# Optimization experiments

Measured on AMD Instinct MI355X. Metric: run time of the kernel, lower is better.

## Reference

```python
import jax, jax.numpy as jnp
import numpy as np

N = 100000
F_IN = 128
HIDDEN = 64
HEADS = 4
EPS = 1e-16
SLOPE = 0.2  # PyG GATConv default negative_slope


def gat_conv(x, src, dst, W, a_src, a_dst, b, heads, out_ch, concat, n_nodes):
    # x: [N, F]; W: [F, heads*out_ch]; a_src/a_dst: [heads, out_ch]
    h = (x @ W).reshape(n_nodes, heads, out_ch)              # [N, H, C]
    alpha_s = jnp.einsum('nhc,hc->nh', h, a_src)             # [N, H]
    alpha_d = jnp.einsum('nhc,hc->nh', h, a_dst)             # [N, H]
    e = alpha_s[src] + alpha_d[dst]                          # [E, H]
    e = jnp.where(e > 0, e, SLOPE * e)                       # leaky_relu
    # segment softmax over destination node
    m = jax.ops.segment_max(e, dst, num_segments=n_nodes)    # [N, H]
    m = jnp.where(jnp.isfinite(m), m, 0.0)                   # empty segments
    ex = jnp.exp(e - m[dst])                                 # [E, H]
    denom = jax.ops.segment_sum(ex, dst, num_segments=n_nodes)  # [N, H]
    alpha = ex / (denom[dst] + EPS)                          # [E, H]
    # weighted scatter-aggregate of source features at destinations
    msg = h[src] * alpha[:, :, None]                         # [E, H, C]
    out = jax.ops.segment_sum(msg, dst, num_segments=n_nodes)  # [N, H, C]
    if concat:
        out = out.reshape(n_nodes, heads * out_ch)
    else:
        out = out.mean(axis=1)
    return out + b


def setup_inputs() -> dict:
    key = jax.random.key(0)
    ks = jax.random.split(key, 12)
    x = jax.random.normal(ks[0], (N, F_IN), dtype=jnp.float32)
    edge_index = jax.random.randint(ks[1], (2, 1600000), 0, N, dtype=jnp.int64)
    s1 = 1.0 / np.sqrt(F_IN)
    s2 = 1.0 / np.sqrt(HIDDEN)
    return {
        'x': x,
        'edge_index': edge_index,
        'W1': jax.random.normal(ks[2], (F_IN, HIDDEN), dtype=jnp.float32) * s1,
        'a_src1': jax.random.normal(ks[3], (HEADS, HIDDEN // HEADS), dtype=jnp.float32) * s2,
        'a_dst1': jax.random.normal(ks[4], (HEADS, HIDDEN // HEADS), dtype=jnp.float32) * s2,
        'b1': jnp.zeros((HIDDEN,), dtype=jnp.float32),
        'W2': jax.random.normal(ks[5], (HIDDEN, HIDDEN), dtype=jnp.float32) * s2,
        'a_src2': jax.random.normal(ks[6], (1, HIDDEN), dtype=jnp.float32) * s2,
        'a_dst2': jax.random.normal(ks[7], (1, HIDDEN), dtype=jnp.float32) * s2,
        'b2': jnp.zeros((HIDDEN,), dtype=jnp.float32),
        'Wc': jax.random.normal(ks[8], (HIDDEN, 1), dtype=jnp.float32) * s2,
        'bc': jnp.zeros((1,), dtype=jnp.float32),
    }


def reference(x, edge_index, W1, a_src1, a_dst1, b1, W2, a_src2, a_dst2, b2, Wc, bc):
    src, dst = edge_index[0], edge_index[1]
    # dropout layers are identity in eval mode
    h = gat_conv(x, src, dst, W1, a_src1, a_dst1, b1,
                 heads=HEADS, out_ch=HIDDEN // HEADS, concat=True, n_nodes=N)
    h = jax.nn.relu(h)
    h = gat_conv(h, src, dst, W2, a_src2, a_dst2, b2,
                 heads=1, out_ch=HIDDEN, concat=False, n_nodes=N)
    h = jax.nn.relu(h)
    return h @ Wc + bc  # [N, 1]
```

## Files before the change

kernel.cpp:

```cpp
#include <hip/hip_runtime.h>
#include <hip/hip_bf16.h>


typedef __hip_bfloat16 bf16;
typedef unsigned short ushort;
typedef unsigned char uchar;
typedef __attribute__((ext_vector_type(8))) short short8;
typedef __attribute__((ext_vector_type(4))) float f32x4;

#define NN 100000
#define EE 1600000
#define BKB 9
#define BKN (1 << BKB)
#define NBK ((NN + BKN - 1) >> BKB)
#define CAP 10240
#define TILE 4096
#define EPT 16
#define NT ((EE + TILE - 1) / TILE)
#define GP 391
#define BN 16
#define CHE 512
#define NGRP (NN / BN)

__device__ __forceinline__ float relu_np(float v) { return (v < 0.f) ? 0.f : v; }
__device__ __forceinline__ float lrelu(float v) { return v > 0.f ? v : 0.2f * v; }
__device__ __forceinline__ ushort f2bf(float f) {
    __hip_bfloat16 h = __float2bfloat16(f);
    return *reinterpret_cast<ushort*>(&h);
}
__device__ __forceinline__ float bf2f(ushort u) {
    unsigned int x = ((unsigned int)u) << 16;
    return __uint_as_float(x);
}

__global__ __launch_bounds__(256) void k_pt(
    const int* __restrict__ src, const int* __restrict__ dst,
    int* __restrict__ gcur, int* __restrict__ pairs,
    const float* __restrict__ W1,
    const float* __restrict__ aS1, const float* __restrict__ aD1,
    const float* __restrict__ W2, const float* __restrict__ aS2,
    const float* __restrict__ aD2,
    ushort* __restrict__ wB16, ushort* __restrict__ wE16,
    ushort* __restrict__ wExt)
{
    __shared__ int lh[4][NBK];
    const int bid = blockIdx.x;
    const int tid = threadIdx.x;

    if (bid < NT) {
        for (int i = tid; i < 4 * NBK; i += 256) ((int*)lh)[i] = 0;
        __syncthreads();
        const int wv = tid >> 6;
        const int e0 = bid * TILE;
        int pk[EPT], bk[EPT], rv[EPT];
        #pragma unroll
        for (int j = 0; j < EPT; ++j) {
            int e = e0 + j * 256 + tid;
            if (e < EE) {
                int d = dst[e];
                bk[j] = d >> BKB;
                pk[j] = src[e] | ((d & (BKN - 1)) << 17);
                rv[j] = atomicAdd(&lh[wv][bk[j]], 1);
            }
        }
        __syncthreads();
        for (int i = tid; i < NBK; i += 256) {
            int c0 = lh[0][i], c1 = lh[1][i], c2 = lh[2][i], c3 = lh[3][i];
            int tot = c0 + c1 + c2 + c3;
            int b = tot ? atomicAdd(&gcur[i], tot) : 0;
            lh[0][i] = b;
            lh[1][i] = b + c0;
            lh[2][i] = b + c0 + c1;
            lh[3][i] = b + c0 + c1 + c2;
        }
        __syncthreads();
        #pragma unroll
        for (int j = 0; j < EPT; ++j) {
            int e = e0 + j * 256 + tid;
            if (e < EE)
                pairs[(size_t)bk[j] * CAP + lh[wv][bk[j]] + rv[j]] = pk[j];
        }
    } else if (bid == NT) {
        for (int i = tid; i < 128 * 64; i += 256) {
            int k = i >> 6, n = i & 63;
            wB16[n * 128 + k] = f2bf(W1[i]);
        }
        for (int i = tid; i < 128 * 16; i += 256) {
            int k = i >> 4, j = i & 15;
            float v = 0.f;
            if (j < 8) {
                int h = j & 3;
                const float* av = (j < 4) ? aS1 : aD1;
                for (int c = 0; c < 16; ++c)
                    v = fmaf(W1[k * 64 + h * 16 + c], av[h * 16 + c], v);
            }
            wE16[j * 128 + k] = f2bf(v);
        }
    } else {
        for (int i = tid; i < 80 * 64; i += 256) {
            int n = i >> 6, k = i & 63;
            float v = 0.f;
            if (n < 64) {
                v = W2[k * 64 + n];
            } else if (n == 64) {
                for (int c = 0; c < 64; ++c) v = fmaf(W2[k * 64 + c], aS2[c], v);
            } else if (n == 65) {
                for (int c = 0; c < 64; ++c) v = fmaf(W2[k * 64 + c], aD2[c], v);
            }
            wExt[i] = f2bf(v);
        }
    }
}

__global__ __launch_bounds__(256) void k_bgg(
    const int* __restrict__ gcur, const int* __restrict__ pairs,
    int* __restrict__ row_ptr, uchar* __restrict__ rcnt,
    int* __restrict__ col,
    const float* __restrict__ x,
    const ushort* __restrict__ wB16, const ushort* __restrict__ wE16,
    ushort* __restrict__ h1, float* __restrict__ as1, float* __restrict__ ad1)
{
    __shared__ int h4[4][BKN];
    __shared__ int sP[256];
    const int bid = blockIdx.x;
    const int tid = threadIdx.x;

    if (bid >= NBK) {
        const int gb = bid - NBK;
        const int w = tid >> 6, lane = tid & 63;
        const int m = lane & 15, quad = lane >> 4;
        const int ntiles = NN >> 4;
        for (int tile = gb * 4 + w; tile < ntiles; tile += GP * 4) {
            const int row0 = tile << 4;
            f32x4 acc[4] = {f32x4{0,0,0,0}, f32x4{0,0,0,0},
                            f32x4{0,0,0,0}, f32x4{0,0,0,0}};
            f32x4 acc5 = {0, 0, 0, 0};
            const float* xp = x + (size_t)(row0 + m) * 128 + quad * 8;
            #pragma unroll
            for (int ks = 0; ks < 128; ks += 32) {
                f32x4 x0 = *(const f32x4*)(xp + ks);
                f32x4 x1 = *(const f32x4*)(xp + ks + 4);
                short8 a;
                #pragma unroll
                for (int j = 0; j < 4; ++j) a[j] = (short)f2bf(x0[j]);
                #pragma unroll
                for (int j = 0; j < 4; ++j) a[4 + j] = (short)f2bf(x1[j]);
                #pragma unroll
                for (int t = 0; t < 4; ++t) {
                    short8 b = *(const short8*)&wB16[(t * 16 + m) * 128 + ks + quad * 8];
                    acc[t] = __builtin_amdgcn_mfma_f32_16x16x32_bf16(a, b, acc[t], 0, 0, 0);
                }
                short8 b5 = *(const short8*)&wE16[m * 128 + ks + quad * 8];
                acc5 = __builtin_amdgcn_mfma_f32_16x16x32_bf16(a, b5, acc5, 0, 0, 0);
            }
            #pragma unroll
            for (int t = 0; t < 4; ++t)
                #pragma unroll
                for (int r = 0; r < 4; ++r)
                    h1[(size_t)(row0 + quad * 4 + r) * 64 + t * 16 + m] = f2bf(acc[t][r]);
            #pragma unroll
            for (int r = 0; r < 4; ++r) {
                int row = row0 + quad * 4 + r;
                if (m < 4) as1[row * 4 + m] = acc5[r];
                else if (m < 8) ad1[row * 4 + (m - 4)] = acc5[r];
            }
        }
        return;
    }

    const int b = bid;
    const int n0 = b << BKB;
    const int wv = tid >> 6;
    const int base = b * CAP, endE = base + gcur[b];

    for (int i = tid; i < 4 * BKN; i += 256) ((int*)h4)[i] = 0;
    __syncthreads();
    for (int i = base + tid; i < endE; i += 256)
        atomicAdd(&h4[wv][pairs[i] >> 17], 1);
    __syncthreads();

    const int na = 2 * tid, nb2 = 2 * tid + 1;
    int c00 = h4[0][na], c01 = h4[1][na], c02 = h4[2][na], c03 = h4[3][na];
    int c10 = h4[0][nb2], c11 = h4[1][nb2], c12 = h4[2][nb2], c13 = h4[3][nb2];
    int a0 = c00 + c01 + c02 + c03;
    int a1 = c10 + c11 + c12 + c13;
    int tot = a0 + a1;
    sP[tid] = tot;
    __syncthreads();
    for (int off = 1; off < 256; off <<= 1) {
        int t = (tid >= off) ? sP[tid - off] : 0;
        __syncthreads();
        sP[tid] += t;
        __syncthreads();
    }
    const int excl = sP[tid] - tot;
    const int c0 = base + excl;
    const int c1 = c0 + a0;
    if (n0 + na < NN) {
        row_ptr[n0 + na] = c0;
        rcnt[n0 + na] = (uchar)a0;
    }
    if (n0 + nb2 < NN) {
        row_ptr[n0 + nb2] = c1;
        rcnt[n0 + nb2] = (uchar)a1;
    }
    h4[0][na] = c0;
    h4[1][na] = c0 + c00;
    h4[2][na] = c0 + c00 + c01;
    h4[3][na] = c0 + c00 + c01 + c02;
    h4[0][nb2] = c1;
    h4[1][nb2] = c1 + c10;
    h4[2][nb2] = c1 + c10 + c11;
    h4[3][nb2] = c1 + c10 + c11 + c12;
    __syncthreads();
    for (int i = base + tid; i < endE; i += 256) {
        int pr = pairs[i];
        int p = atomicAdd(&h4[wv][pr >> 17], 1);
        col[p] = pr & 0x1FFFF;
    }
}

__global__ __launch_bounds__(256, 8) void k_seg1f(
    const int* __restrict__ rp, const uchar* __restrict__ rcnt,
    const int* __restrict__ col,
    const float* __restrict__ as1, const float* __restrict__ ad1,
    const ushort* __restrict__ h1, const float* __restrict__ b1,
    const ushort* __restrict__ wExt,
    ushort* __restrict__ h2, float* __restrict__ as2, float* __restrict__ ad2)
{
    __shared__ __align__(16) ushort zS[BN * 72];
    __shared__ float pS[CHE * 4];
    __shared__ int colS[CHE];
    __shared__ uchar ndS[CHE];
    __shared__ int sRp[BN + 1];
    __shared__ float bS[64];
    __shared__ float adS[BN * 4];

    const int tid = threadIdx.x;
    const int n0 = blockIdx.x * BN;

    if (tid < 64) bS[tid] = b1[tid];
    if (tid < BN * 4) adS[tid] = ad1[(size_t)n0 * 4 + tid];
    if (tid < BN) sRp[tid] = rp[n0 + tid];
    if (tid == BN) sRp[BN] = rp[n0 + BN - 1] + (int)rcnt[n0 + BN - 1];
    __syncthreads();

    const int eb0 = sRp[0];
    const int cnt = min(sRp[BN] - eb0, CHE);

    for (int t = tid; t < cnt; t += 256) {
        int ge = eb0 + t;
        colS[t] = col[ge];
        int nd = 0;
        #pragma unroll
        for (int k = 1; k < BN; ++k) nd += (ge >= sRp[k]);
        ndS[t] = (uchar)nd;
    }
    __syncthreads();
    for (int t = tid; t < cnt * 4; t += 256) {
        int e = t >> 2, hh = t & 3;
        float v = as1[(size_t)colS[e] * 4 + hh] + adS[ndS[e] * 4 + hh];
        pS[t] = __expf(lrelu(v));
    }
    __syncthreads();

    const int w = tid >> 6, lane = tid & 63;
    const int g = lane >> 4, c4 = lane & 15, head = c4 >> 2;
    const int nb = w * 4 + g;
    const int s_n = sRp[nb] - eb0, e_n = sRp[nb + 1] - eb0;

    f32x4 acc = {0, 0, 0, 0};
    float den = 0.f;
    int i = s_n;
    for (; i + 3 < e_n; i += 4) {
        int cA = colS[i], cB = colS[i + 1], cC = colS[i + 2], cD = colS[i + 3];
        ushort4 hA = *(const ushort4*)&h1[(size_t)cA * 64 + c4 * 4];
        ushort4 hB = *(const ushort4*)&h1[(size_t)cB * 64 + c4 * 4];
        ushort4 hC = *(const ushort4*)&h1[(size_t)cC * 64 + c4 * 4];
        ushort4 hD = *(const ushort4*)&h1[(size_t)cD * 64 + c4 * 4];
        float pA = pS[(i + 0) * 4 + head], pB = pS[(i + 1) * 4 + head];
        float pC = pS[(i + 2) * 4 + head], pD = pS[(i + 3) * 4 + head];
        den += (pA + pB) + (pC + pD);
        acc[0] = fmaf(pA, bf2f(hA.x), acc[0]);
        acc[1] = fmaf(pA, bf2f(hA.y), acc[1]);
        acc[2] = fmaf(pA, bf2f(hA.z), acc[2]);
        acc[3] = fmaf(pA, bf2f(hA.w), acc[3]);
        acc[0] = fmaf(pB, bf2f(hB.x), acc[0]);
        acc[1] = fmaf(pB, bf2f(hB.y), acc[1]);
        acc[2] = fmaf(pB, bf2f(hB.z), acc[2]);
        acc[3] = fmaf(pB, bf2f(hB.w), acc[3]);
        acc[0] = fmaf(pC, bf2f(hC.x), acc[0]);
        acc[1] = fmaf(pC, bf2f(hC.y), acc[1]);
        acc[2] = fmaf(pC, bf2f(hC.z), acc[2]);
        acc[3] = fmaf(pC, bf2f(hC.w), acc[3]);
        acc[0] = fmaf(pD, bf2f(hD.x), acc[0]);
        acc[1] = fmaf(pD, bf2f(hD.y), acc[1]);
        acc[2] = fmaf(pD, bf2f(hD.z), acc[2]);
        acc[3] = fmaf(pD, bf2f(hD.w), acc[3]);
    }
    for (; i < e_n; ++i) {
        int cA = colS[i];
        ushort4 hA = *(const ushort4*)&h1[(size_t)cA * 64 + c4 * 4];
        float pA = pS[i * 4 + head];
        den += pA;
        acc[0] = fmaf(pA, bf2f(hA.x), acc[0]);
        acc[1] = fmaf(pA, bf2f(hA.y), acc[1]);
        acc[2] = fmaf(pA, bf2f(hA.z), acc[2]);
        acc[3] = fmaf(pA, bf2f(hA.w), acc[3]);
    }
    {
        float inv = 1.f / (den + 1e-16f);
        ushort4 zv;
        zv.x = f2bf(relu_np(acc[0] * inv + bS[c4 * 4 + 0]));
        zv.y = f2bf(relu_np(acc[1] * inv + bS[c4 * 4 + 1]));
        zv.z = f2bf(relu_np(acc[2] * inv + bS[c4 * 4 + 2]));
        zv.w = f2bf(relu_np(acc[3] * inv + bS[c4 * 4 + 3]));
        *(ushort4*)&zS[nb * 72 + c4 * 4] = zv;
    }
    __syncthreads();

    const int m = c4, quad = g;
    for (int t = w; t < 5; t += 4) {
        f32x4 acct = {0, 0, 0, 0};
        #pragma unroll
        for (int ks = 0; ks < 64; ks += 32) {
            short8 a = *(const short8*)&zS[m * 72 + ks + quad * 8];
            short8 b = *(const short8*)&wExt[(t * 16 + m) * 64 + ks + quad * 8];
            acct = __builtin_amdgcn_mfma_f32_16x16x32_bf16(a, b, acct, 0, 0, 0);
        }
        if (t < 4) {
            #pragma unroll
            for (int r = 0; r < 4; ++r)
                h2[(size_t)(n0 + quad * 4 + r) * 64 + t * 16 + m] = f2bf(acct[r]);
        } else {
            #pragma unroll
            for (int r = 0; r < 4; ++r) {
                int row = n0 + quad * 4 + r;
                if (m == 0) as2[row] = acct[r];
                else if (m == 1) ad2[row] = acct[r];
            }
        }
    }
}

__global__ __launch_bounds__(256, 8) void k_seg2f(
    const int* __restrict__ rp, const uchar* __restrict__ rcnt,
    const int* __restrict__ col,
    const float* __restrict__ as2, const float* __restrict__ ad2,
    const ushort* __restrict__ h2, const float* __restrict__ b2,
    const float* __restrict__ Wc, const float* __restrict__ bc,
    float* __restrict__ out)
{
    __shared__ float pS[CHE];
    __shared__ int colS[CHE];
    __shared__ uchar ndS[CHE];
    __shared__ int sRp[BN + 1];
    __shared__ float adS[BN];
    __shared__ float b2S[64];
    __shared__ float wcS[64];

    const int tid = threadIdx.x;
    const int n0 = blockIdx.x * BN;
    if (tid < 64) { b2S[tid] = b2[tid]; wcS[tid] = Wc[tid]; }
    if (tid < BN) { sRp[tid] = rp[n0 + tid]; adS[tid] = ad2[n0 + tid]; }
    if (tid == BN) sRp[BN] = rp[n0 + BN - 1] + (int)rcnt[n0 + BN - 1];
    __syncthreads();

    const int eb0 = sRp[0];
    const int cnt = min(sRp[BN] - eb0, CHE);
    for (int t = tid; t < cnt; t += 256) {
        int ge = eb0 + t;
        colS[t] = col[ge];
        int nd = 0;
        #pragma unroll
        for (int k = 1; k < BN; ++k) nd += (ge >= sRp[k]);
        ndS[t] = (uchar)nd;
    }
    __syncthreads();
    for (int t = tid; t < cnt; t += 256)
        pS[t] = __expf(lrelu(as2[colS[t]] + adS[ndS[t]]));
    __syncthreads();

    const int w = tid >> 6, lane = tid & 63;
    const int g = lane >> 4, c4 = lane & 15;
    const int nb = w * 4 + g;
    const int myn = n0 + nb;
    const int s_n = sRp[nb] - eb0, e_n = sRp[nb + 1] - eb0;

    f32x4 acc = {0, 0, 0, 0};
    float den = 0.f;
    int i = s_n;
    for (; i + 3 < e_n; i += 4) {
        int cA = colS[i], cB = colS[i + 1], cC = colS[i + 2], cD = colS[i + 3];
        ushort4 hA = *(const ushort4*)&h2[(size_t)cA * 64 + c4 * 4];
        ushort4 hB = *(const ushort4*)&h2[(size_t)cB * 64 + c4 * 4];
        ushort4 hC = *(const ushort4*)&h2[(size_t)cC * 64 + c4 * 4];
        ushort4 hD = *(const ushort4*)&h2[(size_t)cD * 64 + c4 * 4];
        float pA = pS[i + 0], pB = pS[i + 1], pC = pS[i + 2], pD = pS[i + 3];
        den += (pA + pB) + (pC + pD);
        acc[0] = fmaf(pA, bf2f(hA.x), acc[0]);
        acc[1] = fmaf(pA, bf2f(hA.y), acc[1]);
        acc[2] = fmaf(pA, bf2f(hA.z), acc[2]);
        acc[3] = fmaf(pA, bf2f(hA.w), acc[3]);
        acc[0] = fmaf(pB, bf2f(hB.x), acc[0]);
        acc[1] = fmaf(pB, bf2f(hB.y), acc[1]);
        acc[2] = fmaf(pB, bf2f(hB.z), acc[2]);
        acc[3] = fmaf(pB, bf2f(hB.w), acc[3]);
        acc[0] = fmaf(pC, bf2f(hC.x), acc[0]);
        acc[1] = fmaf(pC, bf2f(hC.y), acc[1]);
        acc[2] = fmaf(pC, bf2f(hC.z), acc[2]);
        acc[3] = fmaf(pC, bf2f(hC.w), acc[3]);
        acc[0] = fmaf(pD, bf2f(hD.x), acc[0]);
        acc[1] = fmaf(pD, bf2f(hD.y), acc[1]);
        acc[2] = fmaf(pD, bf2f(hD.z), acc[2]);
        acc[3] = fmaf(pD, bf2f(hD.w), acc[3]);
    }
    for (; i < e_n; ++i) {
        int cA = colS[i];
        ushort4 hA = *(const ushort4*)&h2[(size_t)cA * 64 + c4 * 4];
        float pA = pS[i];
        den += pA;
        acc[0] = fmaf(pA, bf2f(hA.x), acc[0]);
        acc[1] = fmaf(pA, bf2f(hA.y), acc[1]);
        acc[2] = fmaf(pA, bf2f(hA.z), acc[2]);
        acc[3] = fmaf(pA, bf2f(hA.w), acc[3]);
    }

    float inv = 1.f / (den + 1e-16f);
    float t2 = 0.f;
    #pragma unroll
    for (int j = 0; j < 4; ++j)
        t2 += relu_np(acc[j] * inv + b2S[c4 * 4 + j]) * wcS[c4 * 4 + j];
    t2 += __shfl_xor(t2, 1);
    t2 += __shfl_xor(t2, 2);
    t2 += __shfl_xor(t2, 4);
    t2 += __shfl_xor(t2, 8);
    if (c4 == 0) out[myn] = t2 + bc[0];
}

extern "C" void kernel_launch(void* const* d_in, const int* in_sizes, int n_in,
                              void* d_out, int out_size, void* d_ws, size_t ws_size,
                              hipStream_t stream)
{
    const float* x   = (const float*)d_in[0];
    const int*   ei  = (const int*)d_in[1];
    const float* W1  = (const float*)d_in[2];
    const float* aS1 = (const float*)d_in[3];
    const float* aD1 = (const float*)d_in[4];
    const float* b1  = (const float*)d_in[5];
    const float* W2  = (const float*)d_in[6];
    const float* aS2 = (const float*)d_in[7];
    const float* aD2 = (const float*)d_in[8];
    const float* b2  = (const float*)d_in[9];
    const float* Wc  = (const float*)d_in[10];
    const float* bc  = (const float*)d_in[11];
    float* out = (float*)d_out;

    const int* src = ei;
    const int* dst = ei + EE;

    ushort* h1   = (ushort*)d_ws;
    ushort* h2   = h1 + (size_t)NN * 64;
    float*  as1  = (float*)(h2 + (size_t)NN * 64);
    float*  ad1  = as1 + (size_t)NN * 4;
    float*  as2  = ad1 + (size_t)NN * 4;
    float*  ad2  = as2 + (size_t)NN;
    ushort* wExt = (ushort*)(ad2 + (size_t)NN);
    ushort* wB16 = wExt + 80 * 64;
    ushort* wE16 = wB16 + 64 * 128;
    int* row_ptr = (int*)(wE16 + 16 * 128);
    uchar* rcnt  = (uchar*)(row_ptr + NN);
    int* gcur    = (int*)(rcnt + ((NN + 3) & ~3));
    int* col     = gcur + NBK;
    int* pairs   = (int*)h2;

    hipMemsetAsync(gcur, 0, NBK * sizeof(int), stream);

    k_pt<<<NT + 2, 256, 0, stream>>>(src, dst, gcur, pairs,
                                     W1, aS1, aD1, W2, aS2, aD2,
                                     wB16, wE16, wExt);

    k_bgg<<<NBK + GP, 256, 0, stream>>>(gcur, pairs, row_ptr, rcnt, col,
                                        x, wB16, wE16, h1, as1, ad1);

    k_seg1f<<<NGRP, 256, 0, stream>>>(row_ptr, rcnt, col, as1, ad1, h1, b1,
                                      wExt, h2, as2, ad2);

    k_seg2f<<<NGRP, 256, 0, stream>>>(row_ptr, rcnt, col, as2, ad2, h2,
                                      b2, Wc, bc, out);
}
```

Measured before the change: 240.5 us.

## Replace global bucket atomics with per-tile local prefix offsets

Each partition tile now runs a block-local exclusive scan over its bucket counts and writes its pairs contiguously inside its own tile region. It records the per-tile bucket offsets in a table, instead of reserving space with global atomics into fixed-capacity bucket slots. The bucket kernel then gathers each bucket's runs from every tile using that table. This removes the global atomics and the memset launch. In exchange the bucket kernel's reads become serial per-run loops with uneven work per thread and a less coalesced access pattern.

Result: slower. 252.3 us (+4.9%).

```diff
diff --git a/kernel.cpp b/kernel.cpp
--- a/kernel.cpp
+++ b/kernel.cpp
@@ -21,6 +21,7 @@
 #define BN 16
 #define CHE 512
 #define NGRP (NN / BN)
+#define LPW (NBK + 1)
 
 __device__ __forceinline__ float relu_np(float v) { return (v < 0.f) ? 0.f : v; }
 __device__ __forceinline__ float lrelu(float v) { return v > 0.f ? v : 0.2f * v; }
@@ -35,7 +36,7 @@
 
 __global__ __launch_bounds__(256) void k_pt(
     const int* __restrict__ src, const int* __restrict__ dst,
-    int* __restrict__ gcur, int* __restrict__ pairs,
+    int* __restrict__ lpre, int* __restrict__ pairs,
     const float* __restrict__ W1,
     const float* __restrict__ aS1, const float* __restrict__ aD1,
     const float* __restrict__ W2, const float* __restrict__ aS2,
@@ -44,6 +45,7 @@
     ushort* __restrict__ wExt)
 {
     __shared__ int lh[4][NBK];
+    __shared__ int sP[256];
     const int bid = blockIdx.x;
     const int tid = threadIdx.x;
 
@@ -64,21 +66,34 @@
             }
         }
         __syncthreads();
-        for (int i = tid; i < NBK; i += 256) {
-            int c0 = lh[0][i], c1 = lh[1][i], c2 = lh[2][i], c3 = lh[3][i];
-            int tot = c0 + c1 + c2 + c3;
-            int b = tot ? atomicAdd(&gcur[i], tot) : 0;
-            lh[0][i] = b;
-            lh[1][i] = b + c0;
-            lh[2][i] = b + c0 + c1;
-            lh[3][i] = b + c0 + c1 + c2;
-        }
+        int c0 = 0, c1 = 0, c2 = 0, c3 = 0, tot = 0;
+        if (tid < NBK) {
+            c0 = lh[0][tid]; c1 = lh[1][tid]; c2 = lh[2][tid]; c3 = lh[3][tid];
+            tot = c0 + c1 + c2 + c3;
+        }
+        sP[tid] = tot;
+        __syncthreads();
+        for (int off = 1; off < 256; off <<= 1) {
+            int t = (tid >= off) ? sP[tid - off] : 0;
+            __syncthreads();
+            sP[tid] += t;
+            __syncthreads();
+        }
+        if (tid < NBK) {
+            int excl = sP[tid] - tot;
+            lh[0][tid] = excl;
+            lh[1][tid] = excl + c0;
+            lh[2][tid] = excl + c0 + c1;
+            lh[3][tid] = excl + c0 + c1 + c2;
+            lpre[bid * LPW + tid] = excl;
+        }
+        if (tid == 0) lpre[bid * LPW + NBK] = sP[255];
         __syncthreads();
         #pragma unroll
         for (int j = 0; j < EPT; ++j) {
             int e = e0 + j * 256 + tid;
             if (e < EE)
-                pairs[(size_t)bk[j] * CAP + lh[wv][bk[j]] + rv[j]] = pk[j];
+                pairs[bid * TILE + lh[wv][bk[j]] + rv[j]] = pk[j];
         }
     } else if (bid == NT) {
         for (int i = tid; i < 128 * 64; i += 256) {
@@ -113,7 +128,7 @@
 }
 
 __global__ __launch_bounds__(256) void k_bgg(
-    const int* __restrict__ gcur, const int* __restrict__ pairs,
+    const int* __restrict__ lpre, const int* __restrict__ pairs,
     int* __restrict__ row_ptr, uchar* __restrict__ rcnt,
     int* __restrict__ col,
     const float* __restrict__ x,
@@ -122,6 +137,8 @@
 {
     __shared__ int h4[4][BKN];
     __shared__ int sP[256];
+    __shared__ int runS[NT];
+    __shared__ int runE[NT];
     const int bid = blockIdx.x;
     const int tid = threadIdx.x;
 
@@ -171,12 +188,19 @@
     const int b = bid;
     const int n0 = b << BKB;
     const int wv = tid >> 6;
-    const int base = b * CAP, endE = base + gcur[b];
-
+    const int base = b * CAP;
+
+    for (int r = tid; r < NT; r += 256) {
+        runS[r] = lpre[r * LPW + b];
+        runE[r] = lpre[r * LPW + b + 1];
+    }
     for (int i = tid; i < 4 * BKN; i += 256) ((int*)h4)[i] = 0;
     __syncthreads();
-    for (int i = base + tid; i < endE; i += 256)
-        atomicAdd(&h4[wv][pairs[i] >> 17], 1);
+    for (int r = tid; r < NT; r += 256) {
+        const int* pp = pairs + r * TILE;
+        for (int j = runS[r]; j < runE[r]; ++j)
+            atomicAdd(&h4[wv][pp[j] >> 17], 1);
+    }
     __syncthreads();
 
     const int na = 2 * tid, nb2 = 2 * tid + 1;
@@ -213,10 +237,13 @@
     h4[2][nb2] = c1 + c10 + c11;
     h4[3][nb2] = c1 + c10 + c11 + c12;
     __syncthreads();
-    for (int i = base + tid; i < endE; i += 256) {
-        int pr = pairs[i];
-        int p = atomicAdd(&h4[wv][pr >> 17], 1);
-        col[p] = pr & 0x1FFFF;
+    for (int r = tid; r < NT; r += 256) {
+        const int* pp = pairs + r * TILE;
+        for (int j = runS[r]; j < runE[r]; ++j) {
+            int pr = pp[j];
+            int p = atomicAdd(&h4[wv][pr >> 17], 1);
+            col[p] = pr & 0x1FFFF;
+        }
     }
 }
 
@@ -470,17 +497,15 @@
     ushort* wE16 = wB16 + 64 * 128;
     int* row_ptr = (int*)(wE16 + 16 * 128);
     uchar* rcnt  = (uchar*)(row_ptr + NN);
-    int* gcur    = (int*)(rcnt + ((NN + 3) & ~3));
-    int* col     = gcur + NBK;
+    int* lpre    = (int*)(rcnt + ((NN + 3) & ~3));
+    int* col     = lpre + NT * LPW;
     int* pairs   = (int*)h2;
 
-    hipMemsetAsync(gcur, 0, NBK * sizeof(int), stream);
-
-    k_pt<<<NT + 2, 256, 0, stream>>>(src, dst, gcur, pairs,
+    k_pt<<<NT + 2, 256, 0, stream>>>(src, dst, lpre, pairs,
                                      W1, aS1, aD1, W2, aS2, aD2,
                                      wB16, wE16, wExt);
 
-    k_bgg<<<NBK + GP, 256, 0, stream>>>(gcur, pairs, row_ptr, rcnt, col,
+    k_bgg<<<NBK + GP, 256, 0, stream>>>(lpre, pairs, row_ptr, rcnt, col,
                                         x, wB16, wE16, h1, as1, ad1);
 
     k_seg1f<<<NGRP, 256, 0, stream>>>(row_ptr, rcnt, col, as1, ad1, h1, b1,
```
